# Kernel tuning notes

Measured on AMD Instinct MI355X. Metric: run time of the kernel, lower is better.

The kernel has to match this reference:

```python
import jax, jax.numpy as jnp
import numpy as np

B, S, D, H, F = 2, 2048, 1024, 16, 4096
DH = D // H


def setup_inputs() -> dict:
    key = jax.random.key(0)
    ks = jax.random.split(key, 8)
    scale = 0.02
    def nrm(k, shape):
        return jax.random.normal(k, shape, jnp.float32) * scale
    return {
        "x": jax.random.normal(ks[0], (B, S, D), jnp.float32),
        "ln1_g": jnp.ones((D,), jnp.float32),
        "ln1_b": jnp.zeros((D,), jnp.float32),
        "wq": nrm(ks[1], (D, D)), "bq": jnp.zeros((D,), jnp.float32),
        "wk": nrm(ks[2], (D, D)), "bk": jnp.zeros((D,), jnp.float32),
        "wv": nrm(ks[3], (D, D)), "bv": jnp.zeros((D,), jnp.float32),
        "wo": nrm(ks[4], (D, D)), "bo": jnp.zeros((D,), jnp.float32),
        "ln2_g": jnp.ones((D,), jnp.float32),
        "ln2_b": jnp.zeros((D,), jnp.float32),
        "w1": nrm(ks[5], (D, F)), "b1": jnp.zeros((F,), jnp.float32),
        "w2": nrm(ks[6], (F, D)), "b2": jnp.zeros((D,), jnp.float32),
    }


def _layernorm(x, g, b, eps=1e-5):
    m = jnp.mean(x, axis=-1, keepdims=True)
    v = jnp.var(x, axis=-1, keepdims=True)
    return (x - m) / jnp.sqrt(v + eps) * g + b


def reference(x, ln1_g, ln1_b, wq, bq, wk, bk, wv, bv, wo, bo,
              ln2_g, ln2_b, w1, b1, w2, b2):
    # GPT2Block forward, prefill path (state=None): K/V = ln_1(x), causal mask.
    Bx, Sx, Dx = x.shape
    h = _layernorm(x, ln1_g, ln1_b)

    def heads(t):  # [B,S,D] -> [B,H,S,DH]
        return t.reshape(Bx, Sx, H, DH).transpose(0, 2, 1, 3)

    q = heads(h @ wq + bq)
    k = heads(h @ wk + bk)
    v = heads(h @ wv + bv)

    scores = jnp.einsum('bhqd,bhkd->bhqk', q, k) / jnp.sqrt(jnp.float32(DH))
    # masked_softmax: key position < valid_len (= query_pos+1) kept; else -1e6
    causal = jnp.arange(Sx)[None, :] <= jnp.arange(Sx)[:, None]  # [S,S]
    scores = jnp.where(causal, scores, jnp.float32(-1e6))
    attn_w = jax.nn.softmax(scores, axis=-1)

    o = jnp.einsum('bhqk,bhkd->bhqd', attn_w, v)
    o = o.transpose(0, 2, 1, 3).reshape(Bx, Sx, Dx)
    attn_out = o @ wo + bo

    add1 = x + attn_out  # dropout inactive (eval)
    h2 = _layernorm(add1, ln2_g, ln2_b)
    mlp = jax.nn.gelu(h2 @ w1 + b1, approximate=False) @ w2 + b2
    return add1 + mlp
```

## Files before the change

kernel.cpp:

```cpp
#include <hip/hip_runtime.h>
#include <hip/hip_bf16.h>


#define BDIM 1024
#define SEQ 2048
#define NH 16
#define DHEAD 64
#define FDIM 4096
#define QKVD 3072

typedef __attribute__((ext_vector_type(8))) short short8v;
typedef __attribute__((ext_vector_type(4))) float floatx4;

__device__ __forceinline__ unsigned short f2bf(float f) {
    unsigned int u = __float_as_uint(f);
    unsigned int r = u + 0x7FFFu + ((u >> 16) & 1u);
    return (unsigned short)(r >> 16);
}
__device__ __forceinline__ unsigned int pack2bf(float a, float b) {
    return (unsigned int)f2bf(a) | ((unsigned int)f2bf(b) << 16);
}

__device__ __forceinline__ void load16_lds(const unsigned short* g, short* l) {
    __builtin_amdgcn_global_load_lds((const __attribute__((address_space(1))) void*)g,
                                     (__attribute__((address_space(3))) void*)l, 16, 0, 0);
}

__global__ __launch_bounds__(256) void transpose_all(const float* __restrict__ wq,
                                                     const float* __restrict__ wk,
                                                     const float* __restrict__ wv,
                                                     const float* __restrict__ wo,
                                                     const float* __restrict__ w1,
                                                     const float* __restrict__ w2,
                                                     unsigned short* __restrict__ qkvT,
                                                     unsigned short* __restrict__ woT,
                                                     unsigned short* __restrict__ w1T,
                                                     unsigned short* __restrict__ w2T) {
    const int g = blockIdx.x;
    const float* W;
    unsigned short* Wt;
    int K, N, tx, ty;
    if (g < 4096) {
        const int w = g >> 10, tile = g & 1023;
        tx = tile & 31; ty = tile >> 5; K = 1024; N = 1024;
        W = (w == 0) ? wq : (w == 1) ? wk : (w == 2) ? wv : wo;
        Wt = (w == 3) ? woT : qkvT + (size_t)w * 1024 * 1024;
    } else if (g < 8192) {
        const int tile = g - 4096;
        tx = tile & 127; ty = tile >> 7; K = 1024; N = 4096;
        W = w1; Wt = w1T;
    } else {
        const int tile = g - 8192;
        tx = tile & 31; ty = tile >> 5; K = 4096; N = 1024;
        W = w2; Wt = w2T;
    }
    __shared__ float tile[32][33];
    const int t = threadIdx.x;
    const int r = t >> 3, c4 = (t & 7) * 4;
    const int n0 = tx * 32, k0 = ty * 32;
    float4 p = *(const float4*)(W + (size_t)(k0 + r) * N + n0 + c4);
    tile[r][c4 + 0] = p.x;
    tile[r][c4 + 1] = p.y;
    tile[r][c4 + 2] = p.z;
    tile[r][c4 + 3] = p.w;
    __syncthreads();
    ushort4 ou;
    ou.x = f2bf(tile[c4 + 0][r]);
    ou.y = f2bf(tile[c4 + 1][r]);
    ou.z = f2bf(tile[c4 + 2][r]);
    ou.w = f2bf(tile[c4 + 3][r]);
    *(ushort4*)(Wt + (size_t)(n0 + r) * K + k0 + c4) = ou;
}

__global__ void concat_bias(const float* __restrict__ a, const float* __restrict__ b,
                            const float* __restrict__ c, float* __restrict__ out) {
    int i = blockIdx.x * 256 + threadIdx.x;
    out[i] = (i < 1024) ? a[i] : (i < 2048 ? b[i - 1024] : c[i - 2048]);
}

__global__ __launch_bounds__(256) void ln_kernel(const float* __restrict__ x,
                                                 const float* __restrict__ g,
                                                 const float* __restrict__ bb,
                                                 unsigned short* __restrict__ out) {
    const int row = blockIdx.x;
    const int t = threadIdx.x;
    const int c = t * 4;
    float4 p = *(const float4*)(x + (size_t)row * BDIM + c);
    float s = p.x + p.y + p.z + p.w;
    float sq = p.x * p.x + p.y * p.y + p.z * p.z + p.w * p.w;
    for (int off = 1; off < 64; off <<= 1) {
        s += __shfl_xor(s, off);
        sq += __shfl_xor(sq, off);
    }
    __shared__ float ssum[4], ssq[4];
    const int wave = t >> 6, lane = t & 63;
    if (lane == 0) { ssum[wave] = s; ssq[wave] = sq; }
    __syncthreads();
    s = ssum[0] + ssum[1] + ssum[2] + ssum[3];
    sq = ssq[0] + ssq[1] + ssq[2] + ssq[3];
    const float mean = s * (1.0f / BDIM);
    const float var = sq * (1.0f / BDIM) - mean * mean;
    const float rstd = rsqrtf(var + 1e-5f);
    float4 gg = *(const float4*)(g + c);
    float4 bv = *(const float4*)(bb + c);
    ushort4 o;
    o.x = f2bf((p.x - mean) * rstd * gg.x + bv.x);
    o.y = f2bf((p.y - mean) * rstd * gg.y + bv.y);
    o.z = f2bf((p.z - mean) * rstd * gg.z + bv.z);
    o.w = f2bf((p.w - mean) * rstd * gg.w + bv.w);
    *(ushort4*)(out + (size_t)row * BDIM + c) = o;
}

template <int BN, int RES, int GELU, int OBF16, int QSCALE = 0, int VOUT = 0>
__global__ __launch_bounds__(256, 3) void mfma_gemm(const unsigned short* __restrict__ A,
                                                    const unsigned short* __restrict__ Bt,
                                                    const float* __restrict__ bias,
                                                    const float* __restrict__ res,
                                                    void* __restrict__ Cv,
                                                    unsigned short* __restrict__ vtout,
                                                    int M, int N, int K) {
    constexpr int MI = (BN == 128) ? 4 : 2;
    constexpr int CHB = BN * 4;
    __shared__ short As[2][128 * 32];
    __shared__ short Bs[2][BN * 32];
    const int t = threadIdx.x;
    const int wave = t >> 6, lane = t & 63;
    const int m0 = blockIdx.y * 128, n0 = blockIdx.x * BN;
    const int wmrow = (BN == 128) ? (wave & 1) * 64 : wave * 32;
    const int wnrow = (BN == 128) ? (wave >> 1) * 64 : 0;
    const int mlane = lane & 15, quad = lane >> 4;

    floatx4 acc[MI][4];
#pragma unroll
    for (int mi = 0; mi < MI; ++mi)
#pragma unroll
        for (int ni = 0; ni < 4; ++ni) {
            floatx4 z = {0.0f, 0.0f, 0.0f, 0.0f};
            acc[mi][ni] = z;
        }

    for (int k0 = 0; k0 < K; k0 += 64) {
        __syncthreads();
#pragma unroll
        for (int j = 0; j < 4; ++j) {
            const int c = j * 256 + t;
            const int hh = c >> 9, cc = c & 511;
            load16_lds(A + (size_t)(m0 + (cc >> 2)) * K + k0 + hh * 32 + (cc & 3) * 8,
                       &As[hh][cc * 8]);
        }
#pragma unroll
        for (int j = 0; j < CHB / 128; ++j) {
            const int c = j * 256 + t;
            const int hh = c / CHB, cc = c % CHB;
            load16_lds(Bt + (size_t)(n0 + (cc >> 2)) * K + k0 + hh * 32 + (cc & 3) * 8,
                       &Bs[hh][cc * 8]);
        }
        __syncthreads();
#pragma unroll
        for (int hh = 0; hh < 2; ++hh) {
            short8v a[MI], b[4];
#pragma unroll
            for (int mi = 0; mi < MI; ++mi)
                a[mi] = *(const short8v*)&As[hh][(wmrow + mi * 16 + mlane) * 32 + quad * 8];
#pragma unroll
            for (int ni = 0; ni < 4; ++ni)
                b[ni] = *(const short8v*)&Bs[hh][(wnrow + ni * 16 + mlane) * 32 + quad * 8];
#pragma unroll
            for (int mi = 0; mi < MI; ++mi)
#pragma unroll
                for (int ni = 0; ni < 4; ++ni)
                    acc[mi][ni] = __builtin_amdgcn_mfma_f32_16x16x32_bf16(a[mi], b[ni], acc[mi][ni], 0, 0, 0);
        }
    }
#pragma unroll
    for (int mi = 0; mi < MI; ++mi) {
#pragma unroll
        for (int ni = 0; ni < 4; ++ni) {
            const int col = n0 + wnrow + ni * 16 + mlane;
            const float bv = bias[col];
            const int row0 = m0 + wmrow + mi * 16 + quad * 4;
            if (VOUT && col >= 2048) {
                const int vd = col - 2048;
                const int bb = row0 >> 11, ss = row0 & 2047;
                uint2 pk;
                pk.x = pack2bf(acc[mi][ni][0] + bv, acc[mi][ni][1] + bv);
                pk.y = pack2bf(acc[mi][ni][2] + bv, acc[mi][ni][3] + bv);
                *(uint2*)(vtout + ((size_t)(bb * NH + (vd >> 6)) * DHEAD + (vd & 63)) * SEQ + ss) = pk;
            } else {
#pragma unroll
                for (int rg = 0; rg < 4; ++rg) {
                    const int row = row0 + rg;
                    float v = acc[mi][ni][rg] + bv;
                    if (RES) v += res[(size_t)row * N + col];
                    if (GELU) v = 0.5f * v * (1.0f + erff(v * 0.70710678118654752f));
                    if (QSCALE && col < 1024) v *= 0.18033688011112042f;
                    if (OBF16)
                        ((unsigned short*)Cv)[(size_t)row * N + col] = f2bf(v);
                    else
                        ((float*)Cv)[(size_t)row * N + col] = v;
                }
            }
        }
    }
}

__global__ __launch_bounds__(512, 4) void attn_kernel(const unsigned short* __restrict__ qkv,
                                                      const unsigned short* __restrict__ vt,
                                                      unsigned short* __restrict__ o) {
    const int g = blockIdx.x;
    const int qt = (g < 256) ? (15 - (g >> 5)) : ((g - 256) >> 5);
    const int hb = g & 31;
    const int h = hb & 15, b = hb >> 4;
    const int t = threadIdx.x;
    const int wave = t >> 6, lane = t & 63;
    const int mlane = lane & 15, quad = lane >> 4;
    const int msw = mlane & 7;
    const int wq0 = qt * 128 + wave * 16;
    const size_t bS = (size_t)b * SEQ;

    __shared__ unsigned short Ks[64][64];
    __shared__ unsigned short Vs[64][64];
    __shared__ __align__(16) unsigned short plds[8][16][64];

    short8v qf0, qf1;
    {
        const unsigned short* qrow = qkv + (bS + wq0 + mlane) * QKVD + h * DHEAD;
        qf0 = *(const short8v*)(qrow + quad * 8);
        qf1 = *(const short8v*)(qrow + 32 + quad * 8);
    }

    const unsigned short* kbase = qkv + bS * QKVD + 1024 + h * DHEAD;
    const unsigned short* vbase = vt + ((size_t)(b * NH + h)) * DHEAD * SEQ;

    const int sr = t >> 3, sc = t & 7;
    const int ssw = (sc ^ (sr & 7)) * 8;
    const unsigned short* kg = kbase + (size_t)sr * QKVD + sc * 8;
    const unsigned short* vg = vbase + (size_t)sr * SEQ + sc * 8;

    floatx4 ot[4];
#pragma unroll
    for (int mt = 0; mt < 4; ++mt) { floatx4 z = {0, 0, 0, 0}; ot[mt] = z; }
    float m_r = -INFINITY, l_r = 0.0f;

    const int kend = wq0 + 16;
    const int kmax = qt * 128 + 128;

    uint4 kr = *(const uint4*)kg;
    uint4 vr = *(const uint4*)vg;

    for (int k0 = 0; k0 < kmax; k0 += 64) {
        *(uint4*)&Ks[sr][ssw] = kr;
        *(uint4*)&Vs[sr][ssw] = vr;
        __syncthreads();
        if (k0 + 64 < kmax) {
            kr = *(const uint4*)(kg + (size_t)(k0 + 64) * QKVD);
            vr = *(const uint4*)(vg + (k0 + 64));
        }
        if (k0 < kend) {
            floatx4 st[4];
#pragma unroll
            for (int kt = 0; kt < 4; ++kt) {
                if (k0 + kt * 16 < kend) {
                    short8v kfa = *(const short8v*)&Ks[kt * 16 + mlane][(quad ^ msw) * 8];
                    short8v kfb = *(const short8v*)&Ks[kt * 16 + mlane][((quad + 4) ^ msw) * 8];
                    floatx4 z = {0, 0, 0, 0};
                    st[kt] = __builtin_amdgcn_mfma_f32_16x16x32_bf16(kfa, qf0, z, 0, 0, 0);
                    st[kt] = __builtin_amdgcn_mfma_f32_16x16x32_bf16(kfb, qf1, st[kt], 0, 0, 0);
                } else {
                    floatx4 mz = {-1e30f, -1e30f, -1e30f, -1e30f};
                    st[kt] = mz;
                }
            }
            if (k0 + 64 >= kend) {
#pragma unroll
                for (int kt = 0; kt < 4; ++kt)
#pragma unroll
                    for (int rg = 0; rg < 4; ++rg)
                        if (k0 + kt * 16 + quad * 4 + rg > wq0 + mlane)
                            st[kt][rg] = -1e30f;
            }
            float tm = st[0][0];
#pragma unroll
            for (int kt = 0; kt < 4; ++kt)
#pragma unroll
                for (int rg = 0; rg < 4; ++rg) tm = fmaxf(tm, st[kt][rg]);
            tm = fmaxf(tm, __shfl_xor(tm, 16));
            tm = fmaxf(tm, __shfl_xor(tm, 32));
            if (!__all(tm <= m_r + 8.0f)) {
                const float newm = fmaxf(m_r, tm);
                const float alpha = exp2f(m_r - newm);
                l_r *= alpha;
#pragma unroll
                for (int mt = 0; mt < 4; ++mt)
#pragma unroll
                    for (int rg = 0; rg < 4; ++rg) ot[mt][rg] *= alpha;
                m_r = newm;
            }
            float p[4][4], psum = 0.0f;
#pragma unroll
            for (int kt = 0; kt < 4; ++kt)
#pragma unroll
                for (int rg = 0; rg < 4; ++rg) {
                    p[kt][rg] = exp2f(st[kt][rg] - m_r);
                    psum += p[kt][rg];
                }
            psum += __shfl_xor(psum, 16);
            psum += __shfl_xor(psum, 32);
            l_r += psum;
            char* prow = (char*)&plds[wave][mlane][0];
#pragma unroll
            for (int kt = 0; kt < 4; ++kt) {
                uint2 pk;
                pk.x = pack2bf(p[kt][0], p[kt][1]);
                pk.y = pack2bf(p[kt][2], p[kt][3]);
                *(uint2*)(prow + ((kt * 32 + quad * 8) ^ (msw << 4))) = pk;
            }
#pragma unroll
            for (int kh = 0; kh < 2; ++kh) {
                if (k0 + kh * 32 < kend) {
                    short8v vf[4];
#pragma unroll
                    for (int mt = 0; mt < 4; ++mt)
                        vf[mt] = *(const short8v*)&Vs[mt * 16 + mlane][(((kh * 4 + quad) ^ msw)) * 8];
                    short8v pf = *(const short8v*)(prow + (((kh * 4 + quad) ^ msw) << 4));
#pragma unroll
                    for (int mt = 0; mt < 4; ++mt)
                        ot[mt] = __builtin_amdgcn_mfma_f32_16x16x32_bf16(vf[mt], pf, ot[mt], 0, 0, 0);
                }
            }
        }
        __syncthreads();
    }

    const float inv = 1.0f / l_r;
    unsigned short* orow = o + (bS + wq0 + mlane) * BDIM + h * DHEAD;
#pragma unroll
    for (int mt = 0; mt < 4; ++mt) {
        uint2 pk;
        pk.x = pack2bf(ot[mt][0] * inv, ot[mt][1] * inv);
        pk.y = pack2bf(ot[mt][2] * inv, ot[mt][3] * inv);
        *(uint2*)(orow + mt * 16 + quad * 4) = pk;
    }
}

extern "C" void kernel_launch(void* const* d_in, const int* in_sizes, int n_in,
                              void* d_out, int out_size, void* d_ws, size_t ws_size,
                              hipStream_t stream) {
    const int M = 2 * SEQ;

    const float* x = (const float*)d_in[0];
    const float* ln1_g = (const float*)d_in[1];
    const float* ln1_b = (const float*)d_in[2];
    const float* wq = (const float*)d_in[3];
    const float* bq = (const float*)d_in[4];
    const float* wk = (const float*)d_in[5];
    const float* bk = (const float*)d_in[6];
    const float* wv = (const float*)d_in[7];
    const float* bv = (const float*)d_in[8];
    const float* wo = (const float*)d_in[9];
    const float* bo = (const float*)d_in[10];
    const float* ln2_g = (const float*)d_in[11];
    const float* ln2_b = (const float*)d_in[12];
    const float* w1 = (const float*)d_in[13];
    const float* b1 = (const float*)d_in[14];
    const float* w2 = (const float*)d_in[15];
    const float* b2 = (const float*)d_in[16];

    char* wsb = (char*)d_ws;
    unsigned short* qkv = (unsigned short*)wsb;
    unsigned short* ffn = (unsigned short*)wsb;
    unsigned short* vt = (unsigned short*)(wsb + (24u << 20));
    unsigned short* hbuf = (unsigned short*)(wsb + (32u << 20));
    float* add1 = (float*)(wsb + (40u << 20));
    unsigned short* h2 = (unsigned short*)(wsb + (56u << 20));
    unsigned short* qkvT = (unsigned short*)(wsb + (64u << 20));
    unsigned short* woT = (unsigned short*)(wsb + (70u << 20));
    unsigned short* w1T = (unsigned short*)(wsb + (72u << 20));
    unsigned short* w2T = (unsigned short*)(wsb + (80u << 20));
    float* bqkv = (float*)(wsb + (88u << 20));

    transpose_all<<<12288, 256, 0, stream>>>(wq, wk, wv, wo, w1, w2, qkvT, woT, w1T, w2T);
    concat_bias<<<12, 256, 0, stream>>>(bq, bk, bv, bqkv);

    ln_kernel<<<M, 256, 0, stream>>>(x, ln1_g, ln1_b, hbuf);

    mfma_gemm<128, 0, 0, 1, 1, 1><<<dim3(QKVD / 128, M / 128), 256, 0, stream>>>(
        hbuf, qkvT, bqkv, nullptr, qkv, vt, M, QKVD, 1024);

    attn_kernel<<<512, 512, 0, stream>>>(qkv, vt, hbuf);

    mfma_gemm<64, 1, 0, 0><<<dim3(1024 / 64, M / 128), 256, 0, stream>>>(
        hbuf, woT, bo, x, add1, nullptr, M, 1024, 1024);

    ln_kernel<<<M, 256, 0, stream>>>(add1, ln2_g, ln2_b, h2);

    mfma_gemm<128, 0, 1, 1><<<dim3(FDIM / 128, M / 128), 256, 0, stream>>>(
        h2, w1T, b1, nullptr, ffn, nullptr, M, FDIM, 1024);

    mfma_gemm<64, 1, 0, 0><<<dim3(1024 / 64, M / 128), 256, 0, stream>>>(
        ffn, w2T, b2, add1, (float*)d_out, nullptr, M, 1024, FDIM);
}
```

Before: 349.2 us.

## Double-buffer GEMM K-loop with async LDS prefetch and vectorize epilogue

Restructures the MFMA GEMM main loop to step K by 32. It alternates two LDS buffers and prefetches the next tile while computing the current one, which drops one barrier per iteration and overlaps global loads with MFMA. The MFMA operands are swapped so each lane holds four consecutive columns. That lets the epilogue use float4 loads for bias and residual and pack its stores into 8- or 16-byte writes instead of scalar ones. In exchange, the V-transpose output becomes four scalar strided stores, and there are more loop iterations with less work each.

```diff
diff --git a/kernel.cpp b/kernel.cpp
--- a/kernel.cpp
+++ b/kernel.cpp
@@ -120,7 +120,6 @@
                                                     unsigned short* __restrict__ vtout,
                                                     int M, int N, int K) {
     constexpr int MI = (BN == 128) ? 4 : 2;
-    constexpr int CHB = BN * 4;
     __shared__ short As[2][128 * 32];
     __shared__ short Bs[2][BN * 32];
     const int t = threadIdx.x;
@@ -139,65 +138,85 @@
             acc[mi][ni] = z;
         }
 
-    for (int k0 = 0; k0 < K; k0 += 64) {
+    auto stage = [&](int buf, int k0) {
+#pragma unroll
+        for (int j = 0; j < 2; ++j) {
+            const int c = j * 256 + t;
+            load16_lds(A + (size_t)(m0 + (c >> 2)) * K + k0 + (c & 3) * 8, &As[buf][c * 8]);
+        }
+#pragma unroll
+        for (int j = 0; j < BN / 64; ++j) {
+            const int c = j * 256 + t;
+            load16_lds(Bt + (size_t)(n0 + (c >> 2)) * K + k0 + (c & 3) * 8, &Bs[buf][c * 8]);
+        }
+    };
+
+    stage(0, 0);
+    const int nt = K >> 5;
+#pragma unroll 2
+    for (int i = 0; i < nt; ++i) {
+        const int buf = i & 1;
         __syncthreads();
-#pragma unroll
-        for (int j = 0; j < 4; ++j) {
-            const int c = j * 256 + t;
-            const int hh = c >> 9, cc = c & 511;
-            load16_lds(A + (size_t)(m0 + (cc >> 2)) * K + k0 + hh * 32 + (cc & 3) * 8,
-                       &As[hh][cc * 8]);
-        }
-#pragma unroll
-        for (int j = 0; j < CHB / 128; ++j) {
-            const int c = j * 256 + t;
-            const int hh = c / CHB, cc = c % CHB;
-            load16_lds(Bt + (size_t)(n0 + (cc >> 2)) * K + k0 + hh * 32 + (cc & 3) * 8,
-                       &Bs[hh][cc * 8]);
-        }
-        __syncthreads();
-#pragma unroll
-        for (int hh = 0; hh < 2; ++hh) {
-            short8v a[MI], b[4];
-#pragma unroll
-            for (int mi = 0; mi < MI; ++mi)
-                a[mi] = *(const short8v*)&As[hh][(wmrow + mi * 16 + mlane) * 32 + quad * 8];
+        if (i + 1 < nt) stage(buf ^ 1, (i + 1) << 5);
+        short8v a[MI], b[4];
+#pragma unroll
+        for (int mi = 0; mi < MI; ++mi)
+            a[mi] = *(const short8v*)&As[buf][(wmrow + mi * 16 + mlane) * 32 + quad * 8];
+#pragma unroll
+        for (int ni = 0; ni < 4; ++ni)
+            b[ni] = *(const short8v*)&Bs[buf][(wnrow + ni * 16 + mlane) * 32 + quad * 8];
+#pragma unroll
+        for (int mi = 0; mi < MI; ++mi)
 #pragma unroll
             for (int ni = 0; ni < 4; ++ni)
-                b[ni] = *(const short8v*)&Bs[hh][(wnrow + ni * 16 + mlane) * 32 + quad * 8];
-#pragma unroll
-            for (int mi = 0; mi < MI; ++mi)
-#pragma unroll
-                for (int ni = 0; ni < 4; ++ni)
-                    acc[mi][ni] = __builtin_amdgcn_mfma_f32_16x16x32_bf16(a[mi], b[ni], acc[mi][ni], 0, 0, 0);
-        }
-    }
+                acc[mi][ni] = __builtin_amdgcn_mfma_f32_16x16x32_bf16(b[ni], a[mi], acc[mi][ni], 0, 0, 0);
+    }
+
 #pragma unroll
     for (int mi = 0; mi < MI; ++mi) {
+        const int row = m0 + wmrow + mi * 16 + mlane;
 #pragma unroll
         for (int ni = 0; ni < 4; ++ni) {
-            const int col = n0 + wnrow + ni * 16 + mlane;
-            const float bv = bias[col];
-            const int row0 = m0 + wmrow + mi * 16 + quad * 4;
-            if (VOUT && col >= 2048) {
-                const int vd = col - 2048;
-                const int bb = row0 >> 11, ss = row0 & 2047;
-                uint2 pk;
-                pk.x = pack2bf(acc[mi][ni][0] + bv, acc[mi][ni][1] + bv);
-                pk.y = pack2bf(acc[mi][ni][2] + bv, acc[mi][ni][3] + bv);
-                *(uint2*)(vtout + ((size_t)(bb * NH + (vd >> 6)) * DHEAD + (vd & 63)) * SEQ + ss) = pk;
+            const int col0 = n0 + wnrow + ni * 16 + quad * 4;
+            const float4 bv4 = *(const float4*)(bias + col0);
+            float v0 = acc[mi][ni][0] + bv4.x;
+            float v1 = acc[mi][ni][1] + bv4.y;
+            float v2 = acc[mi][ni][2] + bv4.z;
+            float v3 = acc[mi][ni][3] + bv4.w;
+            if (VOUT && col0 >= 2048) {
+                const int vd0 = col0 - 2048;
+                const int bb = row >> 11, ss = row & 2047;
+                unsigned short* vp =
+                    vtout + ((size_t)(bb * NH + (vd0 >> 6)) * DHEAD + (vd0 & 63)) * SEQ + ss;
+                vp[0 * SEQ] = f2bf(v0);
+                vp[1 * SEQ] = f2bf(v1);
+                vp[2 * SEQ] = f2bf(v2);
+                vp[3 * SEQ] = f2bf(v3);
             } else {
-#pragma unroll
-                for (int rg = 0; rg < 4; ++rg) {
-                    const int row = row0 + rg;
-                    float v = acc[mi][ni][rg] + bv;
-                    if (RES) v += res[(size_t)row * N + col];
-                    if (GELU) v = 0.5f * v * (1.0f + erff(v * 0.70710678118654752f));
-                    if (QSCALE && col < 1024) v *= 0.18033688011112042f;
-                    if (OBF16)
-                        ((unsigned short*)Cv)[(size_t)row * N + col] = f2bf(v);
-                    else
-                        ((float*)Cv)[(size_t)row * N + col] = v;
+                if (RES) {
+                    const float4 r4 = *(const float4*)(res + (size_t)row * N + col0);
+                    v0 += r4.x; v1 += r4.y; v2 += r4.z; v3 += r4.w;
+                }
+                if (GELU) {
+                    v0 = 0.5f * v0 * (1.0f + erff(v0 * 0.70710678118654752f));
+                    v1 = 0.5f * v1 * (1.0f + erff(v1 * 0.70710678118654752f));
+                    v2 = 0.5f * v2 * (1.0f + erff(v2 * 0.70710678118654752f));
+                    v3 = 0.5f * v3 * (1.0f + erff(v3 * 0.70710678118654752f));
+                }
+                if (QSCALE && col0 < 1024) {
+                    v0 *= 0.18033688011112042f;
+                    v1 *= 0.18033688011112042f;
+                    v2 *= 0.18033688011112042f;
+                    v3 *= 0.18033688011112042f;
+                }
+                if (OBF16) {
+                    uint2 pk;
+                    pk.x = pack2bf(v0, v1);
+                    pk.y = pack2bf(v2, v3);
+                    *(uint2*)((unsigned short*)Cv + (size_t)row * N + col0) = pk;
+                } else {
+                    float4 o4 = {v0, v1, v2, v3};
+                    *(float4*)((float*)Cv + (size_t)row * N + col0) = o4;
                 }
             }
         }
```

After: 375.4 us. +7.5%, slower.

## Swap MFMA operands for vectorized row-contiguous epilogue and remap workgroups across XCDs

Applied to the files above, without the earlier changes.

Adds a SWAP template path that feeds B then A to the MFMA, so each lane holds four consecutive output columns of one row. The epilogue can then use float4 bias and residual loads and packed bf16 or float4 stores instead of scalar strided accesses. It also remaps the workgroup index in groups of eight, likely so neighbouring tiles land on the same XCD and share L2. The QKV GEMM keeps the old epilogue because of its V-transpose and Q-scale outputs, though it still gets the remapping. The remapping assumes the block count divides by eight.

```diff
diff --git a/kernel.cpp b/kernel.cpp
--- a/kernel.cpp
+++ b/kernel.cpp
@@ -111,7 +111,7 @@
     *(ushort4*)(out + (size_t)row * BDIM + c) = o;
 }
 
-template <int BN, int RES, int GELU, int OBF16, int QSCALE = 0, int VOUT = 0>
+template <int BN, int RES, int GELU, int OBF16, int QSCALE = 0, int VOUT = 0, int SWAP = 1>
 __global__ __launch_bounds__(256, 3) void mfma_gemm(const unsigned short* __restrict__ A,
                                                     const unsigned short* __restrict__ Bt,
                                                     const float* __restrict__ bias,
@@ -125,7 +125,13 @@
     __shared__ short Bs[2][BN * 32];
     const int t = threadIdx.x;
     const int wave = t >> 6, lane = t & 63;
-    const int m0 = blockIdx.y * 128, n0 = blockIdx.x * BN;
+
+    const int nwg = gridDim.x * gridDim.y;
+    int bid = blockIdx.y * gridDim.x + blockIdx.x;
+    bid = (bid & 7) * (nwg >> 3) + (bid >> 3);
+    const int bx = bid % gridDim.x, by = bid / gridDim.x;
+    const int m0 = by * 128, n0 = bx * BN;
+
     const int wmrow = (BN == 128) ? (wave & 1) * 64 : wave * 32;
     const int wnrow = (BN == 128) ? (wave >> 1) * 64 : 0;
     const int mlane = lane & 15, quad = lane >> 4;
@@ -168,36 +174,76 @@
 #pragma unroll
             for (int mi = 0; mi < MI; ++mi)
 #pragma unroll
-                for (int ni = 0; ni < 4; ++ni)
-                    acc[mi][ni] = __builtin_amdgcn_mfma_f32_16x16x32_bf16(a[mi], b[ni], acc[mi][ni], 0, 0, 0);
-        }
-    }
-#pragma unroll
-    for (int mi = 0; mi < MI; ++mi) {
-#pragma unroll
-        for (int ni = 0; ni < 4; ++ni) {
-            const int col = n0 + wnrow + ni * 16 + mlane;
-            const float bv = bias[col];
-            const int row0 = m0 + wmrow + mi * 16 + quad * 4;
-            if (VOUT && col >= 2048) {
-                const int vd = col - 2048;
-                const int bb = row0 >> 11, ss = row0 & 2047;
-                uint2 pk;
-                pk.x = pack2bf(acc[mi][ni][0] + bv, acc[mi][ni][1] + bv);
-                pk.y = pack2bf(acc[mi][ni][2] + bv, acc[mi][ni][3] + bv);
-                *(uint2*)(vtout + ((size_t)(bb * NH + (vd >> 6)) * DHEAD + (vd & 63)) * SEQ + ss) = pk;
-            } else {
-#pragma unroll
-                for (int rg = 0; rg < 4; ++rg) {
-                    const int row = row0 + rg;
-                    float v = acc[mi][ni][rg] + bv;
-                    if (RES) v += res[(size_t)row * N + col];
-                    if (GELU) v = 0.5f * v * (1.0f + erff(v * 0.70710678118654752f));
-                    if (QSCALE && col < 1024) v *= 0.18033688011112042f;
-                    if (OBF16)
-                        ((unsigned short*)Cv)[(size_t)row * N + col] = f2bf(v);
+                for (int ni = 0; ni < 4; ++ni) {
+                    if (SWAP)
+                        acc[mi][ni] = __builtin_amdgcn_mfma_f32_16x16x32_bf16(b[ni], a[mi], acc[mi][ni], 0, 0, 0);
                     else
-                        ((float*)Cv)[(size_t)row * N + col] = v;
+                        acc[mi][ni] = __builtin_amdgcn_mfma_f32_16x16x32_bf16(a[mi], b[ni], acc[mi][ni], 0, 0, 0);
+                }
+        }
+    }
+
+    if (SWAP) {
+#pragma unroll
+        for (int mi = 0; mi < MI; ++mi) {
+            const int row = m0 + wmrow + mi * 16 + mlane;
+#pragma unroll
+            for (int ni = 0; ni < 4; ++ni) {
+                const int col0 = n0 + wnrow + ni * 16 + quad * 4;
+                const float4 bv4 = *(const float4*)(bias + col0);
+                float v0 = acc[mi][ni][0] + bv4.x;
+                float v1 = acc[mi][ni][1] + bv4.y;
+                float v2 = acc[mi][ni][2] + bv4.z;
+                float v3 = acc[mi][ni][3] + bv4.w;
+                if (RES) {
+                    const float4 r4 = *(const float4*)(res + (size_t)row * N + col0);
+                    v0 += r4.x; v1 += r4.y; v2 += r4.z; v3 += r4.w;
+                }
+                if (GELU) {
+                    v0 = 0.5f * v0 * (1.0f + erff(v0 * 0.70710678118654752f));
+                    v1 = 0.5f * v1 * (1.0f + erff(v1 * 0.70710678118654752f));
+                    v2 = 0.5f * v2 * (1.0f + erff(v2 * 0.70710678118654752f));
+                    v3 = 0.5f * v3 * (1.0f + erff(v3 * 0.70710678118654752f));
+                }
+                if (OBF16) {
+                    uint2 pk;
+                    pk.x = pack2bf(v0, v1);
+                    pk.y = pack2bf(v2, v3);
+                    *(uint2*)((unsigned short*)Cv + (size_t)row * N + col0) = pk;
+                } else {
+                    float4 o4 = {v0, v1, v2, v3};
+                    *(float4*)((float*)Cv + (size_t)row * N + col0) = o4;
+                }
+            }
+        }
+    } else {
+#pragma unroll
+        for (int mi = 0; mi < MI; ++mi) {
+#pragma unroll
+            for (int ni = 0; ni < 4; ++ni) {
+                const int col = n0 + wnrow + ni * 16 + mlane;
+                const float bv = bias[col];
+                const int row0 = m0 + wmrow + mi * 16 + quad * 4;
+                if (VOUT && col >= 2048) {
+                    const int vd = col - 2048;
+                    const int bb = row0 >> 11, ss = row0 & 2047;
+                    uint2 pk;
+                    pk.x = pack2bf(acc[mi][ni][0] + bv, acc[mi][ni][1] + bv);
+                    pk.y = pack2bf(acc[mi][ni][2] + bv, acc[mi][ni][3] + bv);
+                    *(uint2*)(vtout + ((size_t)(bb * NH + (vd >> 6)) * DHEAD + (vd & 63)) * SEQ + ss) = pk;
+                } else {
+#pragma unroll
+                    for (int rg = 0; rg < 4; ++rg) {
+                        const int row = row0 + rg;
+                        float v = acc[mi][ni][rg] + bv;
+                        if (RES) v += res[(size_t)row * N + col];
+                        if (GELU) v = 0.5f * v * (1.0f + erff(v * 0.70710678118654752f));
+                        if (QSCALE && col < 1024) v *= 0.18033688011112042f;
+                        if (OBF16)
+                            ((unsigned short*)Cv)[(size_t)row * N + col] = f2bf(v);
+                        else
+                            ((float*)Cv)[(size_t)row * N + col] = v;
+                    }
                 }
             }
         }
@@ -384,19 +430,19 @@
 
     ln_kernel<<<M, 256, 0, stream>>>(x, ln1_g, ln1_b, hbuf);
 
-    mfma_gemm<128, 0, 0, 1, 1, 1><<<dim3(QKVD / 128, M / 128), 256, 0, stream>>>(
+    mfma_gemm<128, 0, 0, 1, 1, 1, 0><<<dim3(QKVD / 128, M / 128), 256, 0, stream>>>(
         hbuf, qkvT, bqkv, nullptr, qkv, vt, M, QKVD, 1024);
 
     attn_kernel<<<512, 512, 0, stream>>>(qkv, vt, hbuf);
 
-    mfma_gemm<64, 1, 0, 0><<<dim3(1024 / 64, M / 128), 256, 0, stream>>>(
+    mfma_gemm<64, 1, 0, 0, 0, 0, 1><<<dim3(1024 / 64, M / 128), 256, 0, stream>>>(
         hbuf, woT, bo, x, add1, nullptr, M, 1024, 1024);
 
     ln_kernel<<<M, 256, 0, stream>>>(add1, ln2_g, ln2_b, h2);
 
-    mfma_gemm<128, 0, 1, 1><<<dim3(FDIM / 128, M / 128), 256, 0, stream>>>(
+    mfma_gemm<128, 0, 1, 1, 0, 0, 1><<<dim3(FDIM / 128, M / 128), 256, 0, stream>>>(
         h2, w1T, b1, nullptr, ffn, nullptr, M, FDIM, 1024);
 
-    mfma_gemm<64, 1, 0, 0><<<dim3(1024 / 64, M / 128), 256, 0, stream>>>(
+    mfma_gemm<64, 1, 0, 0, 0, 0, 1><<<dim3(1024 / 64, M / 128), 256, 0, stream>>>(
         ffn, w2T, b2, add1, (float*)d_out, nullptr, M, 1024, FDIM);
 }
```

Result: slower. 360.2 us (+3.1%).
